# Kernel tuning notes

Measured on AMD Instinct MI355X. Metric: run time of the kernel, lower is better.

Reference implementation:

```python
import jax, jax.numpy as jnp
import numpy as np

C = 8          # n_features
D = 256        # grid side
N = 1_000_000  # query points
K = 27         # kernel**3 neighborhood
OUTPUT_SCALE = 1.0


def _linear_params(key, fin, fout):
    kw, kb = jax.random.split(key)
    s = 1.0 / np.sqrt(fin)
    W = jax.random.uniform(kw, (fin, fout), jnp.float32, -s, s)
    b = jax.random.uniform(kb, (fout,), jnp.float32, -s, s)
    return W, b


def setup_inputs() -> dict:
    key = jax.random.key(0)
    ks = jax.random.split(key, 10)
    points = jax.random.uniform(ks[0], (N, 3), jnp.float32, 0.0, float(D - 1))
    grid = jax.random.normal(ks[1], (1, C, D, D, D), dtype=jnp.float32)
    Wc, bc = _linear_params(ks[2], K * C, C)
    W1, b1 = _linear_params(ks[3], 2 * C, 32)
    W2, b2 = _linear_params(ks[4], C + 32, 16)
    W3, b3 = _linear_params(ks[5], C + 16, 8)
    W4, b4 = _linear_params(ks[6], C + 8, C)
    Ws, bs = _linear_params(ks[7], C, 1)
    Wo, bo = _linear_params(ks[8], C, 1)
    return dict(points=points, grid=grid, Wc=Wc, bc=bc, W1=W1, b1=b1,
                W2=W2, b2=b2, W3=W3, b3=b3, W4=W4, b4=b4,
                Ws=Ws, bs=bs, Wo=Wo, bo=bo)


def _layernorm(z):
    # elementwise_affine=False, eps=1e-5, over last dim
    m = jnp.mean(z, axis=-1, keepdims=True)
    v = jnp.var(z, axis=-1, keepdims=True)
    return (z - m) * jax.lax.rsqrt(v + 1e-5)


def reference(points, grid, Wc, bc, W1, b1, W2, b2, W3, b3, W4, b4, Ws, bs, Wo, bo):
    act = jnp.tanh  # config.RENDERER.activation = torch.nn.Tanh()
    pad = 1  # kernel // 2
    # ReplicationPad3d on (1,C,D,H,W)
    g = jnp.pad(grid[0], ((0, 0), (pad, pad), (pad, pad), (pad, pad)), mode='edge')  # (C, D+2, D+2, D+2)
    pts = points + pad
    idx = jnp.floor(pts).astype(jnp.int32)  # (N,3)
    # 27-neighborhood offsets in loop order i,j,k in range(-1,2)
    r = jnp.arange(-1, 2)
    off = jnp.stack(jnp.meshgrid(r, r, r, indexing='ij'), axis=-1).reshape(K, 3)
    nb = idx[:, None, :] + off[None].astype(jnp.int32)  # (N,27,3)
    feat = g[:, nb[..., 0], nb[..., 1], nb[..., 2]]  # (C, N, 27)
    feat = jnp.transpose(feat, (1, 2, 0))            # (N, 27, C) point-major, neighbor, channel
    cen = g[:, idx[:, 0], idx[:, 1], idx[:, 2]].T    # (N, C)
    # use_count_renderer: normalize last channel (count) by global max
    max_count = jnp.maximum(jnp.max(feat[..., -1]), jnp.max(cen[:, -1])) + 1e-9
    feat = jnp.concatenate([feat[..., :-1], feat[..., -1:] / max_count], axis=-1)
    cen = jnp.concatenate([cen[:, :-1], cen[:, -1:] / max_count], axis=-1)
    x = feat.reshape(feat.shape[0], K * C)  # matches torch contiguous view (neighbor-then-channel)
    # DenseNet-style tiny MLP chain (Dropout2d is identity in eval)
    ctx = act(_layernorm(x @ Wc + bc))
    h = act(jnp.concatenate([cen, ctx], axis=1) @ W1 + b1)
    h = act(jnp.concatenate([cen, h], axis=1) @ W2 + b2)
    h = act(jnp.concatenate([cen, h], axis=1) @ W3 + b3)
    h = act(jnp.concatenate([cen, h], axis=1) @ W4 + b4)
    sdf = OUTPUT_SCALE * jnp.tanh(h @ Ws + bs)
    occ = jax.nn.sigmoid(h @ Wo + bo)
    return jnp.concatenate([sdf, occ], axis=1)  # (N, 2)
```

## Files before the change

kernel.cpp:

```cpp
#include <hip/hip_runtime.h>
#include <hip/hip_fp16.h>

typedef unsigned int u32;
typedef unsigned short u16;

__device__ __forceinline__ u32 encf(float f){ u32 u=__float_as_uint(f); return (u&0x80000000u)? ~u : (u|0x80000000u); }
__device__ __forceinline__ float decf(u32 u){ return (u&0x80000000u)? __uint_as_float(u&0x7fffffffu) : __uint_as_float(~u); }

__device__ __forceinline__ float fast_tanh(float x){
  x = fminf(fmaxf(x, -15.f), 15.f);
  float e = __expf(2.f*x);
  return (e - 1.f) * __builtin_amdgcn_rcpf(e + 1.f);
}
__device__ __forceinline__ float fast_sigmoid(float x){
  x = fminf(fmaxf(x, -15.f), 15.f);
  return __builtin_amdgcn_rcpf(1.f + __expf(-x));
}

__device__ __forceinline__ int base_ix(float p){
  return (int)floorf(p + 1.0f) - 1;
}

__global__ __launch_bounds__(256) void repack16(const float* __restrict__ g,
                                                uint4* __restrict__ rg,
                                                u16* __restrict__ zd){
  u32 v = blockIdx.x*256u + threadIdx.x;
  float c0 = g[v];
  float c1 = g[(1u<<24)+v];
  float c2 = g[(2u<<24)+v];
  float c3 = g[(3u<<24)+v];
  float c4 = g[(4u<<24)+v];
  float c5 = g[(5u<<24)+v];
  float c6 = g[(6u<<24)+v];
  float c7 = g[(7u<<24)+v];
  __half2 p0 = __floats2half2_rn(c0,c1);
  __half2 p1 = __floats2half2_rn(c2,c3);
  __half2 p2 = __floats2half2_rn(c4,c5);
  __half2 p3 = __floats2half2_rn(c6,c7);
  uint4 o;
  o.x = *(const u32*)&p0; o.y = *(const u32*)&p1;
  o.z = *(const u32*)&p2; o.w = *(const u32*)&p3;
  rg[v] = o;
  u32 z = v & 255u;
  const float* g7 = g + ((size_t)7u<<24);
  float zm = g7[z==0u   ? v : v-1u];
  float zp = g7[z==255u ? v : v+1u];
  float m = fmaxf(zm, fmaxf(c7, zp));
  zd[v] = __half_as_ushort(__float2half_rn(m));
}

__global__ __launch_bounds__(256) void ydil(const u16* __restrict__ zd,
                                            u16* __restrict__ yd){
  u32 v = blockIdx.x*256u + threadIdx.x;
  u32 y = (v>>8) & 255u;
  float a = __half2float(__ushort_as_half(zd[y==0u   ? v : v-256u]));
  float b = __half2float(__ushort_as_half(zd[v]));
  float c = __half2float(__ushort_as_half(zd[y==255u ? v : v+256u]));
  float m = fmaxf(a, fmaxf(b, c));
  yd[v] = __half_as_ushort(__float2half_rn(m));
}

__global__ __launch_bounds__(256) void xdil(const u16* __restrict__ yd,
                                            u16* __restrict__ xd){
  u32 v = blockIdx.x*256u + threadIdx.x;
  u32 x = v>>16;
  float a = __half2float(__ushort_as_half(yd[x==0u   ? v : v-65536u]));
  float b = __half2float(__ushort_as_half(yd[v]));
  float c = __half2float(__ushort_as_half(yd[x==255u ? v : v+65536u]));
  float m = fmaxf(a, fmaxf(b, c));
  xd[v] = __half_as_ushort(__float2half_rn(m));
}

__global__ __launch_bounds__(256) void kmax_pt(const float* __restrict__ pts,
                                               const u16* __restrict__ xd,
                                               u32* __restrict__ wmax, int n){
  __shared__ float red[4];
  float m = -3.0e38f;
  for (int i = blockIdx.x*blockDim.x + threadIdx.x; i < n; i += gridDim.x*blockDim.x){
    int ix = base_ix(pts[3*i]);
    int iy = base_ix(pts[3*i+1]);
    int iz = base_ix(pts[3*i+2]);
    u32 cb = ((u32)ix<<16) | ((u32)iy<<8) | (u32)iz;
    m = fmaxf(m, __half2float(__ushort_as_half(xd[cb])));
  }
  #pragma unroll
  for (int o=32;o>=1;o>>=1) m = fmaxf(m, __shfl_xor(m, o));
  int wid = threadIdx.x >> 6;
  if ((threadIdx.x & 63)==0) red[wid] = m;
  __syncthreads();
  if (threadIdx.x == 0){
    float r = fmaxf(fmaxf(red[0],red[1]), fmaxf(red[2],red[3]));
    atomicMax(wmax, encf(r));
  }
}

__device__ __forceinline__ void mlp_tail(const float* __restrict__ cen,
                                         const float* __restrict__ acc0,
                                         float2* __restrict__ out, int i,
                                         const float* __restrict__ W1, const float* __restrict__ b1,
                                         const float* __restrict__ W2, const float* __restrict__ b2,
                                         const float* __restrict__ W3, const float* __restrict__ b3,
                                         const float* __restrict__ W4, const float* __restrict__ b4,
                                         const float* __restrict__ Ws, const float* __restrict__ bs,
                                         const float* __restrict__ Wo, const float* __restrict__ bo)
{
  float mean = 0.f;
  #pragma unroll
  for (int j=0;j<8;j++) mean += acc0[j];
  mean *= 0.125f;
  float var = 0.f;
  #pragma unroll
  for (int j=0;j<8;j++){ float t = acc0[j]-mean; var += t*t; }
  var *= 0.125f;
  float rs = rsqrtf(var + 1e-5f);
  float ctx[8];
  #pragma unroll
  for (int j=0;j<8;j++) ctx[j] = fast_tanh((acc0[j]-mean)*rs);

  float h1[32];
  #pragma unroll
  for (int j=0;j<32;j++){
    float s = b1[j];
    #pragma unroll
    for (int c=0;c<8;c++) s = fmaf(cen[c], W1[c*32 + j], s);
    #pragma unroll
    for (int c=0;c<8;c++) s = fmaf(ctx[c], W1[(8+c)*32 + j], s);
    h1[j] = fast_tanh(s);
  }
  float h2[16];
  #pragma unroll
  for (int j=0;j<16;j++){
    float s = b2[j];
    #pragma unroll
    for (int c=0;c<8;c++) s = fmaf(cen[c], W2[c*16 + j], s);
    #pragma unroll
    for (int c=0;c<32;c++) s = fmaf(h1[c], W2[(8+c)*16 + j], s);
    h2[j] = fast_tanh(s);
  }
  float h3[8];
  #pragma unroll
  for (int j=0;j<8;j++){
    float s = b3[j];
    #pragma unroll
    for (int c=0;c<8;c++) s = fmaf(cen[c], W3[c*8 + j], s);
    #pragma unroll
    for (int c=0;c<16;c++) s = fmaf(h2[c], W3[(8+c)*8 + j], s);
    h3[j] = fast_tanh(s);
  }
  float h4[8];
  #pragma unroll
  for (int j=0;j<8;j++){
    float s = b4[j];
    #pragma unroll
    for (int c=0;c<8;c++) s = fmaf(cen[c], W4[c*8 + j], s);
    #pragma unroll
    for (int c=0;c<8;c++) s = fmaf(h3[c], W4[(8+c)*8 + j], s);
    h4[j] = fast_tanh(s);
  }
  float ssdf = bs[0];
  float socc = bo[0];
  #pragma unroll
  for (int c=0;c<8;c++){
    ssdf = fmaf(h4[c], Ws[c], ssdf);
    socc = fmaf(h4[c], Wo[c], socc);
  }
  out[i] = make_float2(fast_tanh(ssdf), fast_sigmoid(socc));
}

__global__ __launch_bounds__(256) void kmain16(const float* __restrict__ pts,
                                               const uint4* __restrict__ rg,
                                               const u32* __restrict__ wmax,
                                               float2* __restrict__ out, int n,
                                               const float* __restrict__ Wc, const float* __restrict__ bc,
                                               const float* __restrict__ W1, const float* __restrict__ b1,
                                               const float* __restrict__ W2, const float* __restrict__ b2,
                                               const float* __restrict__ W3, const float* __restrict__ b3,
                                               const float* __restrict__ W4, const float* __restrict__ b4,
                                               const float* __restrict__ Ws, const float* __restrict__ bs,
                                               const float* __restrict__ Wo, const float* __restrict__ bo)
{
  int i = blockIdx.x*256 + threadIdx.x;
  if (i >= n) return;
  float inv = 1.0f / (decf(*wmax) + 1e-9f);

  int ix = base_ix(pts[3*i]);
  int iy = base_ix(pts[3*i+1]);
  int iz = base_ix(pts[3*i+2]);
  int xs[3] = {max(ix-1,0), ix, min(ix+1,255)};
  int ys[3] = {max(iy-1,0), iy, min(iy+1,255)};
  int zs[3] = {max(iz-1,0), iz, min(iz+1,255)};

  float cen[8];
  float acc[8];
  #pragma unroll
  for (int j=0;j<8;j++) acc[j] = bc[j];

  #pragma unroll
  for (int a=0;a<3;a++)
  #pragma unroll
  for (int b=0;b<3;b++)
  #pragma unroll
  for (int d=0;d<3;d++){
    const int kk = (a*3+b)*3+d;
    u32 vb = ((u32)xs[a]<<16) | ((u32)ys[b]<<8) | (u32)zs[d];
    uint4 q = rg[vb];
    float2 f0 = __half22float2(*(const __half2*)&q.x);
    float2 f1 = __half22float2(*(const __half2*)&q.y);
    float2 f2 = __half22float2(*(const __half2*)&q.z);
    float2 f3 = __half22float2(*(const __half2*)&q.w);
    float v[8] = {f0.x,f0.y,f1.x,f1.y,f2.x,f2.y,f3.x, f3.y*inv};
    if (kk == 13){
      #pragma unroll
      for (int c=0;c<8;c++) cen[c] = v[c];
    }
    #pragma unroll
    for (int c=0;c<8;c++)
      #pragma unroll
      for (int j=0;j<8;j++)
        acc[j] = fmaf(v[c], Wc[(kk*8+c)*8 + j], acc[j]);
  }

  mlp_tail(cen, acc, out, i, W1,b1,W2,b2,W3,b3,W4,b4,Ws,bs,Wo,bo);
}

__global__ __launch_bounds__(256) void kmax_direct(const float* __restrict__ pts,
                                                   const float* __restrict__ g7,
                                                   u32* __restrict__ wmax, int n){
  float m = -3.0e38f;
  for (int i = blockIdx.x*blockDim.x + threadIdx.x; i < n; i += gridDim.x*blockDim.x){
    int ix = base_ix(pts[3*i]);
    int iy = base_ix(pts[3*i+1]);
    int iz = base_ix(pts[3*i+2]);
    int xs[3] = {max(ix-1,0), ix, min(ix+1,255)};
    int ys[3] = {max(iy-1,0), iy, min(iy+1,255)};
    int zs[3] = {max(iz-1,0), iz, min(iz+1,255)};
    #pragma unroll
    for (int a=0;a<3;a++)
    #pragma unroll
    for (int b=0;b<3;b++){
      u32 rb = ((u32)xs[a]<<16) | ((u32)ys[b]<<8);
      #pragma unroll
      for (int d=0;d<3;d++) m = fmaxf(m, g7[rb + (u32)zs[d]]);
    }
  }
  #pragma unroll
  for (int o=32;o>=1;o>>=1) m = fmaxf(m, __shfl_xor(m, o));
  if ((threadIdx.x & 63)==0) atomicMax(wmax, encf(m));
}

__global__ __launch_bounds__(256) void kmain_direct(const float* __restrict__ pts,
                                                    const float* __restrict__ g,
                                                    const u32* __restrict__ wmax,
                                                    float2* __restrict__ out, int n,
                                                    const float* __restrict__ Wc, const float* __restrict__ bc,
                                                    const float* __restrict__ W1, const float* __restrict__ b1,
                                                    const float* __restrict__ W2, const float* __restrict__ b2,
                                                    const float* __restrict__ W3, const float* __restrict__ b3,
                                                    const float* __restrict__ W4, const float* __restrict__ b4,
                                                    const float* __restrict__ Ws, const float* __restrict__ bs,
                                                    const float* __restrict__ Wo, const float* __restrict__ bo)
{
  int i = blockIdx.x*256 + threadIdx.x;
  if (i >= n) return;
  float inv = 1.0f / (decf(*wmax) + 1e-9f);

  int ix = base_ix(pts[3*i]);
  int iy = base_ix(pts[3*i+1]);
  int iz = base_ix(pts[3*i+2]);
  int xs[3] = {max(ix-1,0), ix, min(ix+1,255)};
  int ys[3] = {max(iy-1,0), iy, min(iy+1,255)};
  int zs[3] = {max(iz-1,0), iz, min(iz+1,255)};

  u32 cb = ((u32)ix<<16) | ((u32)iy<<8) | (u32)iz;
  float cen[8];
  #pragma unroll
  for (int c=0;c<8;c++) cen[c] = g[((u32)c<<24) + cb];
  cen[7] *= inv;

  float acc[8];
  #pragma unroll
  for (int j=0;j<8;j++) acc[j] = bc[j];

  #pragma unroll
  for (int a=0;a<3;a++)
  #pragma unroll
  for (int b=0;b<3;b++)
  #pragma unroll
  for (int d=0;d<3;d++){
    const int kk = (a*3+b)*3+d;
    u32 vb = ((u32)xs[a]<<16) | ((u32)ys[b]<<8) | (u32)zs[d];
    float v[8];
    #pragma unroll
    for (int c=0;c<8;c++) v[c] = g[((u32)c<<24) + vb];
    v[7] *= inv;
    #pragma unroll
    for (int c=0;c<8;c++)
      #pragma unroll
      for (int j=0;j<8;j++)
        acc[j] = fmaf(v[c], Wc[(kk*8+c)*8 + j], acc[j]);
  }

  mlp_tail(cen, acc, out, i, W1,b1,W2,b2,W3,b3,W4,b4,Ws,bs,Wo,bo);
}

extern "C" void kernel_launch(void* const* d_in, const int* in_sizes, int n_in,
                              void* d_out, int out_size, void* d_ws, size_t ws_size,
                              hipStream_t stream)
{
  const float* pts  = (const float*)d_in[0];
  const float* grid = (const float*)d_in[1];
  int n = in_sizes[0] / 3;

  const size_t NV       = (size_t)1 << 24;
  const size_t RG_BYTES = NV * 16;
  const size_t SL_BYTES = NV * 2;
  const size_t NEED     = RG_BYTES + 3*SL_BYTES + 64;

  if (ws_size >= NEED){
    char* base = (char*)d_ws;
    uint4* rg  = (uint4*)base;
    u16*   zd  = (u16*)(base + RG_BYTES);
    u16*   yd  = (u16*)(base + RG_BYTES + SL_BYTES);
    u16*   xd  = (u16*)(base + RG_BYTES + 2*SL_BYTES);
    u32*   wmax= (u32*)(base + RG_BYTES + 3*SL_BYTES);

    hipMemsetAsync(wmax, 0, 64, stream);
    repack16<<<65536, 256, 0, stream>>>(grid, rg, zd);
    ydil<<<65536, 256, 0, stream>>>(zd, yd);
    xdil<<<65536, 256, 0, stream>>>(yd, xd);
    kmax_pt<<<2048, 256, 0, stream>>>(pts, xd, wmax, n);
    kmain16<<<(n+255)/256, 256, 0, stream>>>(pts, rg, wmax, (float2*)d_out, n,
        (const float*)d_in[2],  (const float*)d_in[3],
        (const float*)d_in[4],  (const float*)d_in[5],
        (const float*)d_in[6],  (const float*)d_in[7],
        (const float*)d_in[8],  (const float*)d_in[9],
        (const float*)d_in[10], (const float*)d_in[11],
        (const float*)d_in[12], (const float*)d_in[13],
        (const float*)d_in[14], (const float*)d_in[15]);
  } else {
    u32* wmax = (u32*)d_ws;
    hipMemsetAsync(wmax, 0, 64, stream);
    kmax_direct<<<2048, 256, 0, stream>>>(pts, grid + ((size_t)7<<24), wmax, n);
    kmain_direct<<<(n+255)/256, 256, 0, stream>>>(pts, grid, wmax, (float2*)d_out, n,
        (const float*)d_in[2],  (const float*)d_in[3],
        (const float*)d_in[4],  (const float*)d_in[5],
        (const float*)d_in[6],  (const float*)d_in[7],
        (const float*)d_in[8],  (const float*)d_in[9],
        (const float*)d_in[10], (const float*)d_in[11],
        (const float*)d_in[12], (const float*)d_in[13],
        (const float*)d_in[14], (const float*)d_in[15]);
  }
}
```

Baseline: 563.8 us.

## Bin query points by 8^3 cells and remap blocks across XCDs for gather locality

Adds a histogram, single-block scan and scatter pass that bins points into 8x8x8 voxel cells, so kmax_pt and kmain16 process spatially clustered points and their 27-neighbor gathers hit cache. kmain16 also remaps block IDs so that consecutive sorted chunks land on the same XCD. Separately, the z and y dilation passes are fused into repack16, dropping one full-grid pass. The cost is three extra kernels, atomics, a 16 MB sorted point buffer, and scattered output writes through the stored original index.

```diff
diff --git a/kernel.cpp b/kernel.cpp
--- a/kernel.cpp
+++ b/kernel.cpp
@@ -23,7 +23,7 @@
 
 __global__ __launch_bounds__(256) void repack16(const float* __restrict__ g,
                                                 uint4* __restrict__ rg,
-                                                u16* __restrict__ zd){
+                                                u16* __restrict__ zy){
   u32 v = blockIdx.x*256u + threadIdx.x;
   float c0 = g[v];
   float c1 = g[(1u<<24)+v];
@@ -42,44 +42,88 @@
   o.z = *(const u32*)&p2; o.w = *(const u32*)&p3;
   rg[v] = o;
   u32 z = v & 255u;
+  u32 y = (v>>8) & 255u;
   const float* g7 = g + ((size_t)7u<<24);
-  float zm = g7[z==0u   ? v : v-1u];
-  float zp = g7[z==255u ? v : v+1u];
-  float m = fmaxf(zm, fmaxf(c7, zp));
-  zd[v] = __half_as_ushort(__float2half_rn(m));
-}
-
-__global__ __launch_bounds__(256) void ydil(const u16* __restrict__ zd,
-                                            u16* __restrict__ yd){
-  u32 v = blockIdx.x*256u + threadIdx.x;
-  u32 y = (v>>8) & 255u;
-  float a = __half2float(__ushort_as_half(zd[y==0u   ? v : v-256u]));
-  float b = __half2float(__ushort_as_half(zd[v]));
-  float c = __half2float(__ushort_as_half(zd[y==255u ? v : v+256u]));
-  float m = fmaxf(a, fmaxf(b, c));
-  yd[v] = __half_as_ushort(__float2half_rn(m));
-}
-
-__global__ __launch_bounds__(256) void xdil(const u16* __restrict__ yd,
+  u32 zm = (z==0u)? v : v-1u;
+  u32 zp = (z==255u)? v : v+1u;
+  float m = -3.0e38f;
+  #pragma unroll
+  for (int dy=-1; dy<=1; ++dy){
+    int yy = (int)y + dy;
+    u32 ro = (yy<0 || yy>255) ? 0u : (u32)(dy*256);
+    u32 b0 = zm + ro, b1 = v + ro, b2 = zp + ro;
+    m = fmaxf(m, fmaxf(g7[b0], fmaxf(g7[b1], g7[b2])));
+  }
+  zy[v] = __half_as_ushort(__float2half_rn(m));
+}
+
+__global__ __launch_bounds__(256) void xdil(const u16* __restrict__ zy,
                                             u16* __restrict__ xd){
   u32 v = blockIdx.x*256u + threadIdx.x;
   u32 x = v>>16;
-  float a = __half2float(__ushort_as_half(yd[x==0u   ? v : v-65536u]));
-  float b = __half2float(__ushort_as_half(yd[v]));
-  float c = __half2float(__ushort_as_half(yd[x==255u ? v : v+65536u]));
+  float a = __half2float(__ushort_as_half(zy[x==0u   ? v : v-65536u]));
+  float b = __half2float(__ushort_as_half(zy[v]));
+  float c = __half2float(__ushort_as_half(zy[x==255u ? v : v+65536u]));
   float m = fmaxf(a, fmaxf(b, c));
   xd[v] = __half_as_ushort(__float2half_rn(m));
 }
 
-__global__ __launch_bounds__(256) void kmax_pt(const float* __restrict__ pts,
+__device__ __forceinline__ u32 cell_id(int ix, int iy, int iz){
+  return ((u32)(ix>>3)<<10) | ((u32)(iy>>3)<<5) | (u32)(iz>>3);
+}
+
+__global__ __launch_bounds__(256) void hist(const float* __restrict__ pts,
+                                            u32* __restrict__ cnt, int n){
+  for (int i = blockIdx.x*blockDim.x + threadIdx.x; i < n; i += gridDim.x*blockDim.x){
+    int ix = base_ix(pts[3*i]);
+    int iy = base_ix(pts[3*i+1]);
+    int iz = base_ix(pts[3*i+2]);
+    atomicAdd(&cnt[cell_id(ix,iy,iz)], 1u);
+  }
+}
+
+__global__ __launch_bounds__(1024) void scan32k(const u32* __restrict__ cnt,
+                                                u32* __restrict__ ofs){
+  __shared__ u32 sums[1024];
+  int t = threadIdx.x;
+  u32 loc[32];
+  u32 s = 0;
+  #pragma unroll
+  for (int k=0;k<32;k++){ loc[k] = cnt[t*32+k]; s += loc[k]; }
+  sums[t] = s;
+  __syncthreads();
+  for (int off=1; off<1024; off<<=1){
+    u32 v = (t>=off)? sums[t-off] : 0u;
+    __syncthreads();
+    sums[t] += v;
+    __syncthreads();
+  }
+  u32 run = (t>0)? sums[t-1] : 0u;
+  #pragma unroll
+  for (int k=0;k<32;k++){ ofs[t*32+k] = run; run += loc[k]; }
+}
+
+__global__ __launch_bounds__(256) void scatter(const float* __restrict__ pts,
+                                               u32* __restrict__ ofs,
+                                               float4* __restrict__ srt, int n){
+  for (int i = blockIdx.x*blockDim.x + threadIdx.x; i < n; i += gridDim.x*blockDim.x){
+    float px = pts[3*i], py = pts[3*i+1], pz = pts[3*i+2];
+    int ix = base_ix(px), iy = base_ix(py), iz = base_ix(pz);
+    u32 r = atomicAdd(&ofs[cell_id(ix,iy,iz)], 1u);
+    srt[r] = make_float4(px, py, pz, __uint_as_float((u32)i));
+  }
+}
+
+__global__ __launch_bounds__(256) void kmax_pt(const float4* __restrict__ srt,
                                                const u16* __restrict__ xd,
                                                u32* __restrict__ wmax, int n){
   __shared__ float red[4];
   float m = -3.0e38f;
   for (int i = blockIdx.x*blockDim.x + threadIdx.x; i < n; i += gridDim.x*blockDim.x){
-    int ix = base_ix(pts[3*i]);
-    int iy = base_ix(pts[3*i+1]);
-    int iz = base_ix(pts[3*i+2]);
+    float4 rec = srt[i];
+    int ix = base_ix(rec.x);
+    int iy = base_ix(rec.y);
+    int iz = base_ix(rec.z);
     u32 cb = ((u32)ix<<16) | ((u32)iy<<8) | (u32)iz;
     m = fmaxf(m, __half2float(__ushort_as_half(xd[cb])));
   }
@@ -167,7 +211,7 @@
   out[i] = make_float2(fast_tanh(ssdf), fast_sigmoid(socc));
 }
 
-__global__ __launch_bounds__(256) void kmain16(const float* __restrict__ pts,
+__global__ __launch_bounds__(256) void kmain16(const float4* __restrict__ srt,
                                                const uint4* __restrict__ rg,
                                                const u32* __restrict__ wmax,
                                                float2* __restrict__ out, int n,
@@ -179,13 +223,20 @@
                                                const float* __restrict__ Ws, const float* __restrict__ bs,
                                                const float* __restrict__ Wo, const float* __restrict__ bo)
 {
-  int i = blockIdx.x*256 + threadIdx.x;
-  if (i >= n) return;
+  u32 nwg = gridDim.x;
+  u32 q = nwg >> 3, r = nwg & 7u;
+  u32 xcd = blockIdx.x & 7u, sub = blockIdx.x >> 3;
+  u32 bid = (xcd < r ? xcd*(q+1u) : r*(q+1u) + (xcd-r)*q) + sub;
+
+  int j = (int)(bid*256u + threadIdx.x);
+  if (j >= n) return;
+  float4 rec = srt[j];
+  int i = (int)__float_as_uint(rec.w);
   float inv = 1.0f / (decf(*wmax) + 1e-9f);
 
-  int ix = base_ix(pts[3*i]);
-  int iy = base_ix(pts[3*i+1]);
-  int iz = base_ix(pts[3*i+2]);
+  int ix = base_ix(rec.x);
+  int iy = base_ix(rec.y);
+  int iz = base_ix(rec.z);
   int xs[3] = {max(ix-1,0), ix, min(ix+1,255)};
   int ys[3] = {max(iy-1,0), iy, min(iy+1,255)};
   int zs[3] = {max(iz-1,0), iz, min(iz+1,255)};
@@ -193,7 +244,7 @@
   float cen[8];
   float acc[8];
   #pragma unroll
-  for (int j=0;j<8;j++) acc[j] = bc[j];
+  for (int jj=0;jj<8;jj++) acc[jj] = bc[jj];
 
   #pragma unroll
   for (int a=0;a<3;a++)
@@ -203,11 +254,11 @@
   for (int d=0;d<3;d++){
     const int kk = (a*3+b)*3+d;
     u32 vb = ((u32)xs[a]<<16) | ((u32)ys[b]<<8) | (u32)zs[d];
-    uint4 q = rg[vb];
-    float2 f0 = __half22float2(*(const __half2*)&q.x);
-    float2 f1 = __half22float2(*(const __half2*)&q.y);
-    float2 f2 = __half22float2(*(const __half2*)&q.z);
-    float2 f3 = __half22float2(*(const __half2*)&q.w);
+    uint4 qv = rg[vb];
+    float2 f0 = __half22float2(*(const __half2*)&qv.x);
+    float2 f1 = __half22float2(*(const __half2*)&qv.y);
+    float2 f2 = __half22float2(*(const __half2*)&qv.z);
+    float2 f3 = __half22float2(*(const __half2*)&qv.w);
     float v[8] = {f0.x,f0.y,f1.x,f1.y,f2.x,f2.y,f3.x, f3.y*inv};
     if (kk == 13){
       #pragma unroll
@@ -216,8 +267,8 @@
     #pragma unroll
     for (int c=0;c<8;c++)
       #pragma unroll
-      for (int j=0;j<8;j++)
-        acc[j] = fmaf(v[c], Wc[(kk*8+c)*8 + j], acc[j]);
+      for (int jj=0;jj<8;jj++)
+        acc[jj] = fmaf(v[c], Wc[(kk*8+c)*8 + jj], acc[jj]);
   }
 
   mlp_tail(cen, acc, out, i, W1,b1,W2,b2,W3,b3,W4,b4,Ws,bs,Wo,bo);
@@ -314,22 +365,29 @@
   const size_t NV       = (size_t)1 << 24;
   const size_t RG_BYTES = NV * 16;
   const size_t SL_BYTES = NV * 2;
-  const size_t NEED     = RG_BYTES + 3*SL_BYTES + 64;
+  const size_t SRT_BYTES= (size_t)n * 16;
+  const size_t CNT_BYTES= 32768 * 4;
+  const size_t NEED     = RG_BYTES + 2*SL_BYTES + SRT_BYTES + 2*CNT_BYTES + 64;
 
   if (ws_size >= NEED){
     char* base = (char*)d_ws;
-    uint4* rg  = (uint4*)base;
-    u16*   zd  = (u16*)(base + RG_BYTES);
-    u16*   yd  = (u16*)(base + RG_BYTES + SL_BYTES);
-    u16*   xd  = (u16*)(base + RG_BYTES + 2*SL_BYTES);
-    u32*   wmax= (u32*)(base + RG_BYTES + 3*SL_BYTES);
-
+    uint4*  rg   = (uint4*)base;
+    u16*    zy   = (u16*)(base + RG_BYTES);
+    u16*    xd   = (u16*)(base + RG_BYTES + SL_BYTES);
+    float4* srt  = (float4*)(base + RG_BYTES + 2*SL_BYTES);
+    u32*    cnt  = (u32*)(base + RG_BYTES + 2*SL_BYTES + SRT_BYTES);
+    u32*    ofs  = (u32*)(base + RG_BYTES + 2*SL_BYTES + SRT_BYTES + CNT_BYTES);
+    u32*    wmax = (u32*)(base + RG_BYTES + 2*SL_BYTES + SRT_BYTES + 2*CNT_BYTES);
+
+    hipMemsetAsync(cnt, 0, CNT_BYTES, stream);
     hipMemsetAsync(wmax, 0, 64, stream);
-    repack16<<<65536, 256, 0, stream>>>(grid, rg, zd);
-    ydil<<<65536, 256, 0, stream>>>(zd, yd);
-    xdil<<<65536, 256, 0, stream>>>(yd, xd);
-    kmax_pt<<<2048, 256, 0, stream>>>(pts, xd, wmax, n);
-    kmain16<<<(n+255)/256, 256, 0, stream>>>(pts, rg, wmax, (float2*)d_out, n,
+    repack16<<<65536, 256, 0, stream>>>(grid, rg, zy);
+    xdil<<<65536, 256, 0, stream>>>(zy, xd);
+    hist<<<2048, 256, 0, stream>>>(pts, cnt, n);
+    scan32k<<<1, 1024, 0, stream>>>(cnt, ofs);
+    scatter<<<2048, 256, 0, stream>>>(pts, ofs, srt, n);
+    kmax_pt<<<2048, 256, 0, stream>>>(srt, xd, wmax, n);
+    kmain16<<<(n+255)/256, 256, 0, stream>>>(srt, rg, wmax, (float2*)d_out, n,
         (const float*)d_in[2],  (const float*)d_in[3],
         (const float*)d_in[4],  (const float*)d_in[5],
         (const float*)d_in[6],  (const float*)d_in[7],
```

New measurement: 541.7 us. 1.04x faster.
